# Optimization experiments

Measured on AMD Instinct MI355X. Metric: run time of the kernel, lower is better.

## Reference

```python
import jax, jax.numpy as jnp
import numpy as np
from jax import lax

MAXHD = 200.0
MAXV = 40.0
MINA = -6.0
MAXA = 4.0
DT = 0.1
PAST = 25
NVEH = 4096
NT = 256


def setup_inputs() -> dict:
    key = jax.random.key(0)
    ks = jax.random.split(key, 8)
    s = 0.1
    return dict(
        lead_states=jax.random.uniform(ks[0], (NVEH, NT + PAST - 1, 2), dtype=jnp.float32),
        cur_states=jax.random.uniform(ks[1], (NVEH, PAST, 2), dtype=jnp.float32),
        mask=jnp.ones((NVEH, NT + PAST - 1), dtype=jnp.float32),
        conv1_w=jax.random.normal(ks[2], (3, 3, 32), dtype=jnp.float32) * s,
        conv1_b=jnp.zeros((32,), dtype=jnp.float32),
        conv2_w=jax.random.normal(ks[3], (3, 32, 64), dtype=jnp.float32) * s,
        conv2_b=jnp.zeros((64,), dtype=jnp.float32),
        dense2_w=jax.random.normal(ks[4], (384, 10), dtype=jnp.float32) * s,
        dense2_b=jnp.zeros((10,), dtype=jnp.float32),
        dense1_w=jax.random.normal(ks[5], (10, 1), dtype=jnp.float32) * s,
        dense1_b=jnp.zeros((1,), dtype=jnp.float32),
        nt=NT,
    )


def reference(lead_states, cur_states, mask, conv1_w, conv1_b, conv2_w, conv2_b,
              dense2_w, dense2_b, dense1_w, dense1_b, nt):
    nveh = lead_states.shape[0]
    lead_pos = lead_states[:, :, 0]      # (nveh, nt+past-1)
    lead_speeds = lead_states[:, :, 1]

    dn = ('NWC', 'WIO', 'NWC')

    def cnn(x):
        # x: (nveh, PAST, 3)
        x = jax.nn.relu(lax.conv_general_dilated(x, conv1_w, (1,), 'SAME', dimension_numbers=dn) + conv1_b)
        x = lax.reduce_window(x, -jnp.inf, lax.max, (1, 2, 1), (1, 2, 1), 'SAME')   # (nveh,13,32)
        x = jax.nn.relu(lax.conv_general_dilated(x, conv2_w, (1,), 'VALID', dimension_numbers=dn) + conv2_b)
        x = lax.reduce_window(x, -jnp.inf, lax.max, (1, 2, 1), (1, 2, 1), 'SAME')   # (nveh,6,64)
        x = x.reshape(x.shape[0], -1)                                               # (nveh,384)
        x = jax.nn.relu(x @ dense2_w + dense2_b)
        x = x @ dense1_w + dense1_b                                                 # (nveh,1)
        return (MAXA - MINA) * x + MINA

    def step(carry, t):
        cur_pos, cur_speeds = carry                    # each (nveh, PAST)
        lp = lax.dynamic_slice(lead_pos, (0, t), (nveh, PAST))
        ls = lax.dynamic_slice(lead_speeds, (0, t), (nveh, PAST))
        x = jnp.stack([(lp - cur_pos) / MAXHD, cur_speeds / MAXV, ls / MAXV], axis=2)
        acc = cnn(x)                                   # (nveh,1)
        pred_pos = cur_pos[:, -1:] + DT * cur_speeds[:, -1:]
        pred_sp = cur_speeds[:, -1:] + DT * acc
        new_pos = jnp.concatenate([cur_pos[:, 1:], pred_pos], axis=1)
        new_sp = jnp.concatenate([cur_speeds[:, 1:], pred_sp], axis=1)
        return (new_pos, new_sp), (pred_pos[:, 0], pred_sp[:, 0])

    init = (cur_states[:, :, 0], cur_states[:, :, 1])
    _, (pos_preds, speed_preds) = lax.scan(step, init, jnp.arange(nt))
    # (nt, nveh) -> (nveh, nt, 2)
    return jnp.stack([pos_preds.T, speed_preds.T], axis=2)
```

## Files before the change

kernel.cpp:

```cpp
#include <hip/hip_runtime.h>
#include <stdint.h>


#define PAST 25
#define NTW_MAX 280

typedef __attribute__((ext_vector_type(8))) short bf16x8;
typedef __attribute__((ext_vector_type(4))) float f32x4;
typedef unsigned short u16x2 __attribute__((ext_vector_type(2)));
#define MFMA16 __builtin_amdgcn_mfma_f32_16x16x32_bf16

static __device__ __forceinline__ uint32_t f2bf(float f) {
  union { float f; uint32_t u; } x; x.f = f;
  return (x.u + 0x7FFFu + ((x.u >> 16) & 1u)) >> 16;
}
static __device__ __forceinline__ float bf2f(uint32_t b) {
  union { uint32_t u; float f; } x; x.u = b << 16; return x.f;
}
static __device__ __forceinline__ uint32_t pkbf(float lo, float hi) {
  uint32_t r;
  asm("v_cvt_pk_bf16_f32 %0, %1, %2" : "=v"(r) : "v"(lo), "v"(hi));
  return r;
}
static __device__ __forceinline__ f32x4 bcast4(float v) { f32x4 r = {v, v, v, v}; return r; }

static __device__ __forceinline__ uint32_t pkmax(uint32_t a, uint32_t b) {
#if __has_builtin(__builtin_elementwise_max)
  union U { uint32_t w; u16x2 v; } x, y; x.w = a; y.w = b;
  x.v = __builtin_elementwise_max(x.v, y.v);
  return x.w;
#else
  uint32_t al = a << 16, bl = b << 16;
  uint32_t lo = (al > bl ? al : bl) >> 16;
  uint32_t ah = a & 0xffff0000u, bh = b & 0xffff0000u;
  uint32_t hi = ah > bh ? ah : bh;
  return lo | hi;
#endif
}
static __device__ __forceinline__ uint4 maxq(uint4 a, uint4 b) {
  uint4 r; r.x = pkmax(a.x, b.x); r.y = pkmax(a.y, b.y);
  r.z = pkmax(a.z, b.z); r.w = pkmax(a.w, b.w); return r;
}
static __device__ __forceinline__ int w21(int x) { if (x >= 21) x -= 21; if (x >= 21) x -= 21; return x; }
static __device__ __forceinline__ int w17(int x) { if (x >= 17) x -= 17; if (x >= 17) x -= 17; return x; }
static __device__ __forceinline__ float rsum16(float x) {
  x += __builtin_bit_cast(float, __builtin_amdgcn_update_dpp(0, __builtin_bit_cast(int, x), 0x121, 0xf, 0xf, true));
  x += __builtin_bit_cast(float, __builtin_amdgcn_update_dpp(0, __builtin_bit_cast(int, x), 0x122, 0xf, 0xf, true));
  x += __builtin_bit_cast(float, __builtin_amdgcn_update_dpp(0, __builtin_bit_cast(int, x), 0x124, 0xf, 0xf, true));
  x += __builtin_bit_cast(float, __builtin_amdgcn_update_dpp(0, __builtin_bit_cast(int, x), 0x128, 0xf, 0xf, true));
  return x;
}

union FragU { bf16x8 v; uint16_t u[8]; uint4 q; };
struct RowD { f32x4 d0, d1; };

struct __align__(16) SMem {
  uint32_t Xcol[8][33][2];
  float    leadx[8][256];
  uint16_t leady[8][256];
  uint16_t P[25 * 8 * 32];
  uint16_t O2[22 * 8 * 64];
  float2 obuf[2][8][32];
  f32x4 JpartA[4][64];
  f32x4 JpartB[4][64];
};

__global__ __launch_bounds__(256, 2) void rnncf_kernel(
    const float* __restrict__ lead_states, const float* __restrict__ cur_states,
    const float* __restrict__ conv1_w, const float* __restrict__ conv1_b,
    const float* __restrict__ conv2_w, const float* __restrict__ conv2_b,
    const float* __restrict__ dense2_w, const float* __restrict__ dense2_b,
    const float* __restrict__ dense1_w, const float* __restrict__ dense1_b,
    float* __restrict__ out, int nt, int ntw) {
  __shared__ SMem sm;
  const int tid = threadIdx.x;
  const int lane = tid & 63;
  const int wid = tid >> 6;
  const int n = lane & 15;
  const int quad = lane >> 4;
  const int vbase = blockIdx.x * 8;
  const int bpidx = ((lane >> 4) << 6) | ((lane & 7) << 2);

  if (tid < 200) {
    int v = tid & 7, u = tid >> 3;
    const float2 l = *(const float2*)(lead_states + ((size_t)(vbase + v) * ntw + u) * 2);
    const float2 c = *(const float2*)(cur_states + ((size_t)(vbase + v) * PAST + u) * 2);
    float x0 = (l.x - c.x) * 0.005f;
    uint32_t w0 = pkbf(x0, c.y * 0.025f);
    sm.Xcol[v][u][0] = w0;
    sm.Xcol[v][u][1] = pkbf(l.y * 0.025f, x0 - bf2f(w0 & 0xffffu));
  }
#pragma unroll
  for (int v = 0; v < 8; ++v)
    for (int i = 25 + tid; i < ntw; i += 256) {
      const float2 l = *(const float2*)(lead_states + ((size_t)(vbase + v) * ntw + i) * 2);
      sm.leadx[v][i - 25] = l.x;
      sm.leady[v][i - 25] = (uint16_t)f2bf(l.y * 0.025f);
    }

  float pos_s = 0.f, spd_s = 0.f;
  if (wid == 3 && quad < 2 && n < 4) {
    int veh = quad * 4 + n;
    const float2 c = *(const float2*)(cur_states + ((size_t)(vbase + veh) * PAST + 24) * 2);
    pos_s = c.x * 0.005f; spd_s = c.y * 0.025f;
  }

  FragU B1[2];
#pragma unroll
  for (int ct = 0; ct < 2; ++ct)
#pragma unroll
    for (int jj = 0; jj < 8; ++jj) {
      int k = quad * 8 + jj;
      int dw = k & 3, cig = (k >> 2) & 3;
      float w = 0.f;
      if (k < 16 && dw < 3) {
        int ci = (cig == 3) ? 0 : cig;
        w = conv1_w[(dw * 3 + ci) * 32 + ct * 16 + n];
      }
      B1[ct].u[jj] = (uint16_t)f2bf(w);
    }
  FragU B2[3][4];
#pragma unroll
  for (int dw = 0; dw < 3; ++dw)
#pragma unroll
    for (int ct = 0; ct < 4; ++ct)
#pragma unroll
      for (int jj = 0; jj < 8; ++jj) {
        int kap = quad * 8 + jj;
        int ci = (kap & 1) * 16 + (kap >> 1);
        B2[dw][ct].u[jj] = (uint16_t)f2bf(conv2_w[(dw * 32 + ci) * 64 + ct * 16 + n]);
      }
  FragU Bd[12];
#pragma unroll
  for (int kt = 0; kt < 12; ++kt)
#pragma unroll
    for (int jj = 0; jj < 8; ++jj) {
      int flat = kt * 32 + quad * 8 + jj;
      int jp = flat >> 6, kap = flat & 63;
      int co = (kap & 3) * 16 + (kap >> 2);
      Bd[kt].u[jj] = (uint16_t)f2bf((n < 10) ? dense2_w[(jp * 64 + co) * 10 + n] : 0.f);
    }
  f32x4 b1q0, b1q1;
#pragma unroll
  for (int r = 0; r < 4; ++r) {
    b1q0[r] = conv1_b[quad * 4 + r];
    b1q1[r] = conv1_b[16 + quad * 4 + r];
  }
  float b2v[4];
#pragma unroll
  for (int ct = 0; ct < 4; ++ct) b2v[ct] = conv2_b[ct * 16 + n];
  const float d2bv = (n < 10) ? dense2_b[n] : 0.f;
  const float wd1v = (n < 10) ? dense1_w[n] : 0.f;
  const float bd1v = dense1_b[0];

  auto pIdx = [&](int s, int veh, int ch) { return ((s * 8 + veh) * 4 + ch) * 8; };
  auto oIdx = [&](int s, int veh, int ch) { return ((s * 8 + veh) * 8 + ch) * 8; };

  auto build_x = [&](int c, int padL, int padR) -> FragU {
    int h = quad & 1, v8 = n & 7;
    uint32_t d0 = padL ? 0u : sm.Xcol[v8][(c - 1) & 31][h];
    uint32_t d1 = sm.Xcol[v8][c & 31][h];
    uint32_t d2 = padR ? 0u : sm.Xcol[v8][(c + 1) & 31][h];
    FragU a;
    a.q.x = __builtin_amdgcn_perm(d1, d0, 0x05040100u);
    a.q.y = d2 & 0xffffu;
    a.q.z = __builtin_amdgcn_perm(d1, d0, 0x07060302u);
    a.q.w = d2 >> 16;
    return a;
  };

  auto conv1s_row = [&](int c, int padL, int padR) -> RowD {
    FragU a = build_x(c, padL, padR);
    RowD rd;
    rd.d0 = MFMA16(B1[0].v, a.v, b1q0, 0, 0, 0);
    rd.d1 = MFMA16(B1[1].v, a.v, b1q1, 0, 0, 0);
    return rd;
  };

  auto relumax4 = [&](const f32x4& a, const f32x4& b) -> f32x4 {
    f32x4 r;
#pragma unroll
    for (int i = 0; i < 4; ++i) r[i] = fmaxf(fmaxf(a[i], b[i]), 0.f);
    return r;
  };
  auto relu4 = [&](const f32x4& a) -> f32x4 {
    f32x4 r;
#pragma unroll
    for (int i = 0; i < 4; ++i) r[i] = fmaxf(a[i], 0.f);
    return r;
  };
  auto pack4 = [&](const f32x4& p0, const f32x4& p1) -> uint4 {
    uint4 w;
    w.x = pkbf(p0[0], p1[0]); w.y = pkbf(p0[1], p1[1]);
    w.z = pkbf(p0[2], p1[2]); w.w = pkbf(p0[3], p1[3]);
    return w;
  };
  auto p_store = [&](const uint4& w, int ds) {
    if (n < 8) *(uint4*)&sm.P[pIdx(ds, n, quad ^ (n & 3))] = w;
  };
  auto pool_store = [&](const RowD& A, const RowD& Bq, int ds) {
    p_store(pack4(relumax4(A.d0, Bq.d0), relumax4(A.d1, Bq.d1)), ds);
  };
  auto bperm_frag = [&](const uint4& w) -> FragU {
    FragU f;
    f.q.x = (uint32_t)__builtin_amdgcn_ds_bpermute(bpidx, (int)w.x);
    f.q.y = (uint32_t)__builtin_amdgcn_ds_bpermute(bpidx, (int)w.y);
    f.q.z = (uint32_t)__builtin_amdgcn_ds_bpermute(bpidx, (int)w.z);
    f.q.w = (uint32_t)__builtin_amdgcn_ds_bpermute(bpidx, (int)w.w);
    return f;
  };

  auto ld_P = [&](int s) -> FragU {
    FragU a; a.q = *(const uint4*)&sm.P[pIdx(s, n & 7, quad ^ (n & 3))]; return a;
  };

  auto conv2_acc = [&](f32x4* acc, int slot, int dw) {
    FragU a = ld_P(slot);
#pragma unroll
    for (int ct = 0; ct < 4; ++ct) acc[ct] = MFMA16(a.v, B2[dw][ct].v, acc[ct], 0, 0, 0);
  };

  auto conv2_accf = [&](f32x4* acc, const FragU& a, int dw) {
#pragma unroll
    for (int ct = 0; ct < 4; ++ct) acc[ct] = MFMA16(a.v, B2[dw][ct].v, acc[ct], 0, 0, 0);
  };

  auto o2_write = [&](const f32x4* acc, int ds) {
    if (quad < 2) {
#pragma unroll
      for (int r = 0; r < 4; ++r) {
        int veh = quad * 4 + r;
        float m0 = fmaxf(acc[0][r], 0.f), m1 = fmaxf(acc[1][r], 0.f);
        float m2 = fmaxf(acc[2][r], 0.f), m3 = fmaxf(acc[3][r], 0.f);
        uint2 w2; w2.x = pkbf(m0, m1); w2.y = pkbf(m2, m3);
        *(uint2*)&sm.O2[oIdx(ds, veh, (n >> 1) ^ (veh & 7)) + (n & 1) * 4] = w2;
      }
    }
  };

  auto dense_jp = [&](int pa, int pb, int jp, f32x4& a0, f32x4& a1) {
#pragma unroll
    for (int hf = 0; hf < 2; ++hf) {
      uint4 qa = *(const uint4*)&sm.O2[oIdx(pa, n & 7, (hf * 4 + quad) ^ (n & 7))];
      if (pb >= 0) {
        uint4 qb = *(const uint4*)&sm.O2[oIdx(pb, n & 7, (hf * 4 + quad) ^ (n & 7))];
        qa = maxq(qa, qb);
      }
      FragU a; a.q = qa;
      if (hf == 0) a0 = MFMA16(a.v, Bd[jp * 2].v, a0, 0, 0, 0);
      else         a1 = MFMA16(a.v, Bd[jp * 2 + 1].v, a1, 0, 0, 0);
    }
  };

  auto dense_jp_pre = [&](int pa, const uint4* qpre, int jp, f32x4& a0, f32x4& a1) {
#pragma unroll
    for (int hf = 0; hf < 2; ++hf) {
      uint4 qa = *(const uint4*)&sm.O2[oIdx(pa, n & 7, (hf * 4 + quad) ^ (n & 7))];
      if (qpre) qa = maxq(qa, qpre[hf]);
      FragU a; a.q = qa;
      if (hf == 0) a0 = MFMA16(a.v, Bd[jp * 2].v, a0, 0, 0, 0);
      else         a1 = MFMA16(a.v, Bd[jp * 2 + 1].v, a1, 0, 0, 0);
    }
  };

  auto flush_out = [&](int bi, int t0, int cnt) {
    int vv = lane >> 3;
    int s0 = (lane & 7) * 4;
#pragma unroll
    for (int kk = 0; kk < 4; ++kk) {
      int s = s0 + kk;
      if (s < cnt) {
        float2 d = sm.obuf[bi][vv][s];
        *(float2*)(out + ((size_t)(vbase + vv) * nt + t0 + s) * 2) = d;
      }
    }
  };

  __syncthreads();

#pragma unroll
  for (int i = 0; i < 5; ++i) {
    int g = 2 + wid + 4 * i;
    RowD A = conv1s_row(g, 0, 0);
    RowD Bq = conv1s_row(g + 1, 0, 0);
    pool_store(A, Bq, g % 21);
  }
  __syncthreads();

#pragma unroll
  for (int i = 0; i < 4; ++i) {
    int a = 2 + wid + 4 * i;
    f32x4 acc[4];
#pragma unroll
    for (int ct = 0; ct < 4; ++ct) acc[ct] = bcast4(b2v[ct]);
    conv2_acc(acc, a % 21, 0);
    conv2_acc(acc, (a + 2) % 21, 1);
    conv2_acc(acc, (a + 4) % 21, 2);
    o2_write(acc, a % 17);
  }
  __syncthreads();

  RowD c1A = {};
  f32x4 accA[4] = {}, accB[4] = {};
  if (wid == 0) {
    RowD A = conv1s_row(0, 1, 0), Bq = conv1s_row(1, 0, 0);
    pool_store(A, Bq, 23);
  } else if (wid == 1) {
    RowD A = conv1s_row(1, 1, 0), Bq = conv1s_row(2, 0, 0);
    pool_store(A, Bq, 24);
  }
  __syncthreads();
  if (wid == 0) {
    f32x4 aj[4];
#pragma unroll
    for (int ct = 0; ct < 4; ++ct) aj[ct] = bcast4(b2v[ct]);
    conv2_acc(aj, 23, 0); conv2_acc(aj, 2, 1); conv2_acc(aj, 4, 2);
    o2_write(aj, 17);
  } else if (wid == 1) {
    f32x4 aj[4];
#pragma unroll
    for (int ct = 0; ct < 4; ++ct) aj[ct] = bcast4(b2v[ct]);
    conv2_acc(aj, 24, 0); conv2_acc(aj, 3, 1); conv2_acc(aj, 5, 2);
    o2_write(aj, 18);
  } else if (wid == 2) {
    RowD A = conv1s_row(4, 1, 0), Bq = conv1s_row(5, 0, 0);
    pool_store(A, Bq, 21);
  } else {
    RowD A = conv1s_row(5, 1, 0), Bq = conv1s_row(6, 0, 0);
    pool_store(A, Bq, 22);
  }
  __syncthreads();
  if (wid == 0) {
    f32x4 a0 = bcast4(d2bv), a1 = bcast4(0.f);
    dense_jp(17, 2, 0, a0, a1);
    dense_jp(4, 6, 1, a0, a1);
    dense_jp(8, 10, 2, a0, a1);
    dense_jp(12, 14, 3, a0, a1);
    sm.JpartA[0][lane] = a0; sm.JpartB[0][lane] = a1;
  } else if (wid == 1) {
    f32x4 a0 = bcast4(d2bv), a1 = bcast4(0.f);
    dense_jp(18, 3, 0, a0, a1);
    dense_jp(5, 7, 1, a0, a1);
    dense_jp(9, 11, 2, a0, a1);
    dense_jp(13, 15, 3, a0, a1);
    sm.JpartA[1][lane] = a0; sm.JpartB[1][lane] = a1;
  } else if (wid == 2) {
    RowD A = conv1s_row(2, 1, 0), Bq = conv1s_row(3, 0, 0);
    pool_store(A, Bq, 23);
  } else {
    RowD A = conv1s_row(3, 1, 0), Bq = conv1s_row(4, 0, 0);
    pool_store(A, Bq, 24);
  }
  __syncthreads();
  if (wid == 0) {
    f32x4 aj[4];
#pragma unroll
    for (int ct = 0; ct < 4; ++ct) aj[ct] = bcast4(b2v[ct]);
    conv2_acc(aj, 23, 0); conv2_acc(aj, 4, 1); conv2_acc(aj, 6, 2);
    o2_write(aj, 19);
  } else if (wid == 1) {
    f32x4 aj[4];
#pragma unroll
    for (int ct = 0; ct < 4; ++ct) aj[ct] = bcast4(b2v[ct]);
    conv2_acc(aj, 24, 0); conv2_acc(aj, 5, 1); conv2_acc(aj, 7, 2);
    o2_write(aj, 20);
  } else if (wid == 3) {
#pragma unroll
    for (int ct = 0; ct < 4; ++ct) accA[ct] = bcast4(b2v[ct]);
    conv2_acc(accA, 18, 0);
    conv2_acc(accA, 20, 1);
#pragma unroll
    for (int ct = 0; ct < 4; ++ct) accB[ct] = bcast4(b2v[ct]);
    conv2_acc(accB, 20, 0);
    c1A = conv1s_row(22, 0, 0);
  }
  __syncthreads();

  if (wid == 3) __builtin_amdgcn_s_setprio(2);

  int tmA21 = 0, tmA17 = 0;
  const int nsup = nt >> 1;
  for (int k = 0; k < nsup; ++k) {
    if (wid == 3) {
#pragma unroll
      for (int d = 0; d < 2; ++d) {
        const int t = 2 * k + d;
        const int sP22 = w21(tmA21 + d + 22);
        const int sO16 = w17(tmA17 + d + 16);
        const int sO18 = w17(tmA17 + d + 18);
        const int sP18n = w21(tmA21 + d + 19);
        const int sP20n = w21(tmA21 + d + 21);
        f32x4 jpA = sm.JpartA[t & 3][lane];
        f32x4 jpB = sm.JpartB[t & 3][lane];
        uint4 qj8[2];
#pragma unroll
        for (int hf = 0; hf < 2; ++hf)
          qj8[hf] = *(const uint4*)&sm.O2[oIdx(sO16, n & 7, (hf * 4 + quad) ^ (n & 7))];
        FragU fA18 = ld_P(sP18n);
        FragU fA20 = ld_P(sP20n);
        RowD Bq = conv1s_row(t + 23, 0, 0);
        RowD Sg = conv1s_row(t + 24, 0, 1);
        uint4 w11 = pack4(relumax4(c1A.d0, Bq.d0), relumax4(c1A.d1, Bq.d1));
        uint4 w12 = pack4(relu4(Sg.d0), relu4(Sg.d1));
        p_store(w11, sP22);
        c1A = Bq;
        FragU f11 = bperm_frag(w11);
        FragU f12 = bperm_frag(w12);
        conv2_accf(accA, f11, 2);
        conv2_accf(accB, f11, 1);
        conv2_accf(accB, f12, 2);
        o2_write(accA, sO18);
        o2_write(accB, 21);
        f32x4 acc2 = bcast4(0.f), acc3 = bcast4(0.f);
        f32x4 acc4 = bcast4(0.f), acc5 = bcast4(0.f);
        dense_jp_pre(sO18, qj8, 4, acc2, acc3);
        dense_jp_pre(21, (const uint4*)nullptr, 5, acc4, acc5);
        float s0 = fmaxf(jpA[0] + jpB[0] + acc2[0] + acc3[0] + acc4[0] + acc5[0], 0.f) * wd1v;
        float s1 = fmaxf(jpA[1] + jpB[1] + acc2[1] + acc3[1] + acc4[1] + acc5[1], 0.f) * wd1v;
        float s2 = fmaxf(jpA[2] + jpB[2] + acc2[2] + acc3[2] + acc4[2] + acc5[2], 0.f) * wd1v;
        float s3 = fmaxf(jpA[3] + jpB[3] + acc2[3] + acc3[3] + acc4[3] + acc5[3], 0.f) * wd1v;
        s0 = rsum16(s0); s1 = rsum16(s1); s2 = rsum16(s2); s3 = rsum16(s3);
        if (quad < 2 && n < 4) {
          int veh = quad * 4 + n;
          float sv = (n == 0) ? s0 : (n == 1) ? s1 : (n == 2) ? s2 : s3;
          float accv = 10.f * (sv + bd1v) - 6.f;
          float np_s = pos_s + 0.02f * spd_s;
          float nsp = spd_s * 40.f + 0.1f * accv;
          pos_s = np_s; spd_s = nsp * 0.025f;
          float2 o2v; o2v.x = np_s * 200.f; o2v.y = nsp;
          sm.obuf[(t >> 5) & 1][veh][t & 31] = o2v;
          int li = t; if (li > ntw - 26) li = ntw - 26;
          float lnx = sm.leadx[veh][li];
          float lny = bf2f(sm.leady[veh][li]);
          float x0 = lnx * 0.005f - np_s;
          uint32_t wlo = pkbf(x0, spd_s);
          sm.Xcol[veh][(t + PAST) & 31][0] = wlo;
          sm.Xcol[veh][(t + PAST) & 31][1] = pkbf(lny, x0 - bf2f(wlo & 0xffffu));
        }
#pragma unroll
        for (int ct = 0; ct < 4; ++ct) accA[ct] = bcast4(b2v[ct]);
        conv2_accf(accA, fA18, 0);
        conv2_accf(accA, fA20, 1);
#pragma unroll
        for (int ct = 0; ct < 4; ++ct) accB[ct] = bcast4(b2v[ct]);
        conv2_accf(accB, fA20, 0);
      }
    } else if (wid == 0) {
#pragma unroll
      for (int e = 0; e < 2; ++e) {
        const int tau = 2 * k + 2 + e;
        f32x4 a0 = bcast4(d2bv), a1 = bcast4(0.f);
        dense_jp(17 + (tau & 3), w17(tmA17 + 4 + e), 0, a0, a1);
        dense_jp(w17(tmA17 + 6 + e), w17(tmA17 + 8 + e), 1, a0, a1);
        dense_jp(w17(tmA17 + 10 + e), w17(tmA17 + 12 + e), 2, a0, a1);
        dense_jp(w17(tmA17 + 14 + e), w17(tmA17 + 16 + e), 3, a0, a1);
        sm.JpartA[tau & 3][lane] = a0;
        sm.JpartB[tau & 3][lane] = a1;
      }
    } else if (wid == 1) {
      if ((k & 15) == 0 && k > 0) {
        int t0 = 2 * k - 32;
        flush_out((t0 >> 5) & 1, t0, 32);
      }
#pragma unroll
      for (int e = 0; e < 2; ++e) {
        const int tau = 2 * k + 4 + e;
        f32x4 aj[4];
#pragma unroll
        for (int ct = 0; ct < 4; ++ct) aj[ct] = bcast4(b2v[ct]);
        conv2_acc(aj, 21 + (tau & 3), 0);
        conv2_acc(aj, w21(tmA21 + 6 + e), 1);
        conv2_acc(aj, w21(tmA21 + 8 + e), 2);
        o2_write(aj, 17 + (tau & 3));
      }
    } else {
#pragma unroll
      for (int f = 0; f < 2; ++f) {
        const int tau = 2 * k + 6 + f;
        RowD A = conv1s_row(tau, 1, 0);
        RowD Bq = conv1s_row(tau + 1, 0, 0);
        pool_store(A, Bq, 21 + (tau & 3));
      }
    }
    __syncthreads();
    tmA21 = w21(tmA21 + 2);
    tmA17 = w17(tmA17 + 2);
  }

  if (wid == 1) {
    int t0 = (nt - 1) & ~31;
    flush_out((t0 >> 5) & 1, t0, nt - t0);
  }
}

extern "C" void kernel_launch(void* const* d_in, const int* in_sizes, int n_in,
                              void* d_out, int out_size, void* d_ws, size_t ws_size,
                              hipStream_t stream) {
  const float* lead = (const float*)d_in[0];
  const float* cur  = (const float*)d_in[1];
  const float* c1w = (const float*)d_in[3];
  const float* c1b = (const float*)d_in[4];
  const float* c2w = (const float*)d_in[5];
  const float* c2b = (const float*)d_in[6];
  const float* d2w = (const float*)d_in[7];
  const float* d2b = (const float*)d_in[8];
  const float* d1w = (const float*)d_in[9];
  const float* d1b = (const float*)d_in[10];
  float* out = (float*)d_out;

  int nveh = in_sizes[1] / (PAST * 2);
  int ntw  = in_sizes[2] / nveh;
  int nt   = ntw - PAST + 1;
  int nblocks = nveh / 8;

  rnncf_kernel<<<nblocks, 256, 0, stream>>>(lead, cur, c1w, c1b, c2w, c2b,
                                            d2w, d2b, d1w, d1b, out, nt, ntw);
}
```

Measured before the change: 390.2 us.

## Process 16 vehicles per block to fill all MFMA rows

Each block now handles 16 vehicles instead of 8, so the 16-row MFMA tiles carry real vehicles in every row instead of half padding. Shared-memory arrays and index math are resized, the bpermute lane-duplication and the quad/n guards are removed, and the grid is halved. Occupancy drops to one block per CU under the new launch bounds, and only 256 blocks are launched, which may leave CUs underused on a 256-CU part.

```diff
diff --git a/kernel.cpp b/kernel.cpp
--- a/kernel.cpp
+++ b/kernel.cpp
@@ -55,17 +55,17 @@
 struct RowD { f32x4 d0, d1; };
 
 struct __align__(16) SMem {
-  uint32_t Xcol[8][33][2];
-  float    leadx[8][256];
-  uint16_t leady[8][256];
-  uint16_t P[25 * 8 * 32];
-  uint16_t O2[22 * 8 * 64];
-  float2 obuf[2][8][32];
+  uint32_t Xcol[16][33][2];
+  float    leadx[16][256];
+  uint16_t leady[16][256];
+  uint16_t P[25 * 16 * 32];
+  uint16_t O2[22 * 16 * 64];
+  float2 obuf[2][16][32];
   f32x4 JpartA[4][64];
   f32x4 JpartB[4][64];
 };
 
-__global__ __launch_bounds__(256, 2) void rnncf_kernel(
+__global__ __launch_bounds__(256, 1) void rnncf_kernel(
     const float* __restrict__ lead_states, const float* __restrict__ cur_states,
     const float* __restrict__ conv1_w, const float* __restrict__ conv1_b,
     const float* __restrict__ conv2_w, const float* __restrict__ conv2_b,
@@ -78,11 +78,10 @@
   const int wid = tid >> 6;
   const int n = lane & 15;
   const int quad = lane >> 4;
-  const int vbase = blockIdx.x * 8;
-  const int bpidx = ((lane >> 4) << 6) | ((lane & 7) << 2);
-
-  if (tid < 200) {
-    int v = tid & 7, u = tid >> 3;
+  const int vbase = blockIdx.x * 16;
+
+  for (int i = tid; i < 16 * PAST; i += 256) {
+    int v = i & 15, u = i >> 4;
     const float2 l = *(const float2*)(lead_states + ((size_t)(vbase + v) * ntw + u) * 2);
     const float2 c = *(const float2*)(cur_states + ((size_t)(vbase + v) * PAST + u) * 2);
     float x0 = (l.x - c.x) * 0.005f;
@@ -91,7 +90,7 @@
     sm.Xcol[v][u][1] = pkbf(l.y * 0.025f, x0 - bf2f(w0 & 0xffffu));
   }
 #pragma unroll
-  for (int v = 0; v < 8; ++v)
+  for (int v = 0; v < 16; ++v)
     for (int i = 25 + tid; i < ntw; i += 256) {
       const float2 l = *(const float2*)(lead_states + ((size_t)(vbase + v) * ntw + i) * 2);
       sm.leadx[v][i - 25] = l.x;
@@ -99,7 +98,7 @@
     }
 
   float pos_s = 0.f, spd_s = 0.f;
-  if (wid == 3 && quad < 2 && n < 4) {
+  if (wid == 3 && n < 4) {
     int veh = quad * 4 + n;
     const float2 c = *(const float2*)(cur_states + ((size_t)(vbase + veh) * PAST + 24) * 2);
     pos_s = c.x * 0.005f; spd_s = c.y * 0.025f;
@@ -153,11 +152,11 @@
   const float wd1v = (n < 10) ? dense1_w[n] : 0.f;
   const float bd1v = dense1_b[0];
 
-  auto pIdx = [&](int s, int veh, int ch) { return ((s * 8 + veh) * 4 + ch) * 8; };
-  auto oIdx = [&](int s, int veh, int ch) { return ((s * 8 + veh) * 8 + ch) * 8; };
+  auto pIdx = [&](int s, int veh, int ch) { return ((s * 16 + veh) * 4 + ch) * 8; };
+  auto oIdx = [&](int s, int veh, int ch) { return ((s * 16 + veh) * 8 + ch) * 8; };
 
   auto build_x = [&](int c, int padL, int padR) -> FragU {
-    int h = quad & 1, v8 = n & 7;
+    int h = quad & 1, v8 = n;
     uint32_t d0 = padL ? 0u : sm.Xcol[v8][(c - 1) & 31][h];
     uint32_t d1 = sm.Xcol[v8][c & 31][h];
     uint32_t d2 = padR ? 0u : sm.Xcol[v8][(c + 1) & 31][h];
@@ -196,22 +195,14 @@
     return w;
   };
   auto p_store = [&](const uint4& w, int ds) {
-    if (n < 8) *(uint4*)&sm.P[pIdx(ds, n, quad ^ (n & 3))] = w;
+    *(uint4*)&sm.P[pIdx(ds, n, quad ^ (n & 3))] = w;
   };
   auto pool_store = [&](const RowD& A, const RowD& Bq, int ds) {
     p_store(pack4(relumax4(A.d0, Bq.d0), relumax4(A.d1, Bq.d1)), ds);
   };
-  auto bperm_frag = [&](const uint4& w) -> FragU {
-    FragU f;
-    f.q.x = (uint32_t)__builtin_amdgcn_ds_bpermute(bpidx, (int)w.x);
-    f.q.y = (uint32_t)__builtin_amdgcn_ds_bpermute(bpidx, (int)w.y);
-    f.q.z = (uint32_t)__builtin_amdgcn_ds_bpermute(bpidx, (int)w.z);
-    f.q.w = (uint32_t)__builtin_amdgcn_ds_bpermute(bpidx, (int)w.w);
-    return f;
-  };
 
   auto ld_P = [&](int s) -> FragU {
-    FragU a; a.q = *(const uint4*)&sm.P[pIdx(s, n & 7, quad ^ (n & 3))]; return a;
+    FragU a; a.q = *(const uint4*)&sm.P[pIdx(s, n, quad ^ (n & 3))]; return a;
   };
 
   auto conv2_acc = [&](f32x4* acc, int slot, int dw) {
@@ -226,24 +217,22 @@
   };
 
   auto o2_write = [&](const f32x4* acc, int ds) {
-    if (quad < 2) {
-#pragma unroll
-      for (int r = 0; r < 4; ++r) {
-        int veh = quad * 4 + r;
-        float m0 = fmaxf(acc[0][r], 0.f), m1 = fmaxf(acc[1][r], 0.f);
-        float m2 = fmaxf(acc[2][r], 0.f), m3 = fmaxf(acc[3][r], 0.f);
-        uint2 w2; w2.x = pkbf(m0, m1); w2.y = pkbf(m2, m3);
-        *(uint2*)&sm.O2[oIdx(ds, veh, (n >> 1) ^ (veh & 7)) + (n & 1) * 4] = w2;
-      }
+#pragma unroll
+    for (int r = 0; r < 4; ++r) {
+      int veh = quad * 4 + r;
+      float m0 = fmaxf(acc[0][r], 0.f), m1 = fmaxf(acc[1][r], 0.f);
+      float m2 = fmaxf(acc[2][r], 0.f), m3 = fmaxf(acc[3][r], 0.f);
+      uint2 w2; w2.x = pkbf(m0, m1); w2.y = pkbf(m2, m3);
+      *(uint2*)&sm.O2[oIdx(ds, veh, (n >> 1) ^ (veh & 7)) + (n & 1) * 4] = w2;
     }
   };
 
   auto dense_jp = [&](int pa, int pb, int jp, f32x4& a0, f32x4& a1) {
 #pragma unroll
     for (int hf = 0; hf < 2; ++hf) {
-      uint4 qa = *(const uint4*)&sm.O2[oIdx(pa, n & 7, (hf * 4 + quad) ^ (n & 7))];
+      uint4 qa = *(const uint4*)&sm.O2[oIdx(pa, n, (hf * 4 + quad) ^ (n & 7))];
       if (pb >= 0) {
-        uint4 qb = *(const uint4*)&sm.O2[oIdx(pb, n & 7, (hf * 4 + quad) ^ (n & 7))];
+        uint4 qb = *(const uint4*)&sm.O2[oIdx(pb, n, (hf * 4 + quad) ^ (n & 7))];
         qa = maxq(qa, qb);
       }
       FragU a; a.q = qa;
@@ -255,7 +244,7 @@
   auto dense_jp_pre = [&](int pa, const uint4* qpre, int jp, f32x4& a0, f32x4& a1) {
 #pragma unroll
     for (int hf = 0; hf < 2; ++hf) {
-      uint4 qa = *(const uint4*)&sm.O2[oIdx(pa, n & 7, (hf * 4 + quad) ^ (n & 7))];
+      uint4 qa = *(const uint4*)&sm.O2[oIdx(pa, n, (hf * 4 + quad) ^ (n & 7))];
       if (qpre) qa = maxq(qa, qpre[hf]);
       FragU a; a.q = qa;
       if (hf == 0) a0 = MFMA16(a.v, Bd[jp * 2].v, a0, 0, 0, 0);
@@ -264,10 +253,10 @@
   };
 
   auto flush_out = [&](int bi, int t0, int cnt) {
-    int vv = lane >> 3;
-    int s0 = (lane & 7) * 4;
-#pragma unroll
-    for (int kk = 0; kk < 4; ++kk) {
+    int vv = lane >> 2;
+    int s0 = (lane & 3) * 8;
+#pragma unroll
+    for (int kk = 0; kk < 8; ++kk) {
       int s = s0 + kk;
       if (s < cnt) {
         float2 d = sm.obuf[bi][vv][s];
@@ -395,7 +384,7 @@
         uint4 qj8[2];
 #pragma unroll
         for (int hf = 0; hf < 2; ++hf)
-          qj8[hf] = *(const uint4*)&sm.O2[oIdx(sO16, n & 7, (hf * 4 + quad) ^ (n & 7))];
+          qj8[hf] = *(const uint4*)&sm.O2[oIdx(sO16, n, (hf * 4 + quad) ^ (n & 7))];
         FragU fA18 = ld_P(sP18n);
         FragU fA20 = ld_P(sP20n);
         RowD Bq = conv1s_row(t + 23, 0, 0);
@@ -404,8 +393,8 @@
         uint4 w12 = pack4(relu4(Sg.d0), relu4(Sg.d1));
         p_store(w11, sP22);
         c1A = Bq;
-        FragU f11 = bperm_frag(w11);
-        FragU f12 = bperm_frag(w12);
+        FragU f11; f11.q = w11;
+        FragU f12; f12.q = w12;
         conv2_accf(accA, f11, 2);
         conv2_accf(accB, f11, 1);
         conv2_accf(accB, f12, 2);
@@ -420,7 +409,7 @@
         float s2 = fmaxf(jpA[2] + jpB[2] + acc2[2] + acc3[2] + acc4[2] + acc5[2], 0.f) * wd1v;
         float s3 = fmaxf(jpA[3] + jpB[3] + acc2[3] + acc3[3] + acc4[3] + acc5[3], 0.f) * wd1v;
         s0 = rsum16(s0); s1 = rsum16(s1); s2 = rsum16(s2); s3 = rsum16(s3);
-        if (quad < 2 && n < 4) {
+        if (n < 4) {
           int veh = quad * 4 + n;
           float sv = (n == 0) ? s0 : (n == 1) ? s1 : (n == 2) ? s2 : s3;
           float accv = 10.f * (sv + bd1v) - 6.f;
@@ -511,7 +500,7 @@
   int nveh = in_sizes[1] / (PAST * 2);
   int ntw  = in_sizes[2] / nveh;
   int nt   = ntw - PAST + 1;
-  int nblocks = nveh / 8;
+  int nblocks = nveh / 16;
 
   rnncf_kernel<<<nblocks, 256, 0, stream>>>(lead, cur, c1w, c1b, c2w, c2b,
                                             d2w, d2b, d1w, d1b, out, nt, ntw);
```

Measured after the change: 389.8 us. About the same (-0.1%).
